# Optimization experiments

Hardware: AMD Instinct MI355X
Metric: run time of the kernel (lower is better)

## Reference

```python
import jax, jax.numpy as jnp
import numpy as np

N = 50000
E = 800000
IN_CH = 128
HID = 32
HEADS = 8
OUT_CH = 64
NEG_SLOPE = 0.2  # PyG GATConv default leaky_relu slope


def setup_inputs() -> dict:
    key = jax.random.key(0)
    ks = jax.random.split(key, 16)
    x = jax.random.normal(ks[0], (N, IN_CH), dtype=jnp.float32)
    edge_index = jax.random.randint(ks[1], (2, E), 0, N, dtype=jnp.int64)
    s = 0.1
    return {
        "x": x,
        "edge_index": edge_index,
        # layer 1: in -> (HEADS, HID), concat
        "W1": jax.random.normal(ks[2], (IN_CH, HEADS * HID), dtype=jnp.float32) * s,
        "att_src1": jax.random.normal(ks[3], (HEADS, HID), dtype=jnp.float32) * s,
        "att_dst1": jax.random.normal(ks[4], (HEADS, HID), dtype=jnp.float32) * s,
        "b1": jnp.zeros((HEADS * HID,), dtype=jnp.float32),
        # layer 2: HEADS*HID -> (HEADS, HID), concat
        "W2": jax.random.normal(ks[5], (HEADS * HID, HEADS * HID), dtype=jnp.float32) * s,
        "att_src2": jax.random.normal(ks[6], (HEADS, HID), dtype=jnp.float32) * s,
        "att_dst2": jax.random.normal(ks[7], (HEADS, HID), dtype=jnp.float32) * s,
        "b2": jnp.zeros((HEADS * HID,), dtype=jnp.float32),
        # layer 3: HEADS*HID -> (1, OUT_CH), no concat (heads=1)
        "W3": jax.random.normal(ks[8], (HEADS * HID, OUT_CH), dtype=jnp.float32) * s,
        "att_src3": jax.random.normal(ks[9], (1, OUT_CH), dtype=jnp.float32) * s,
        "att_dst3": jax.random.normal(ks[10], (1, OUT_CH), dtype=jnp.float32) * s,
        "b3": jnp.zeros((OUT_CH,), dtype=jnp.float32),
    }


def gat_conv(x, src, dst, W, a_src, a_dst, b, heads, ch, concat):
    n = x.shape[0]
    h = (x @ W).reshape(n, heads, ch)                      # [N,H,C]
    alpha_src = jnp.sum(h * a_src, axis=-1)                # [N,H]
    alpha_dst = jnp.sum(h * a_dst, axis=-1)                # [N,H]
    logits = jax.nn.leaky_relu(alpha_src[src] + alpha_dst[dst], NEG_SLOPE)  # [E,H]
    # numerically stable softmax over edges grouped by destination node
    m = jax.ops.segment_max(logits, dst, num_segments=n)   # [N,H]
    m = jnp.where(jnp.isfinite(m), m, 0.0)
    e = jnp.exp(logits - m[dst])                           # [E,H]
    denom = jax.ops.segment_sum(e, dst, num_segments=n)    # [N,H]
    alpha = e / (denom[dst] + 1e-16)                       # [E,H]
    # weighted scatter-aggregate of source features
    out = jax.ops.segment_sum(alpha[:, :, None] * h[src], dst, num_segments=n)  # [N,H,C]
    out = out.reshape(n, heads * ch) if concat else out.mean(axis=1)
    return out + b


def reference(x, edge_index, W1, att_src1, att_dst1, b1,
              W2, att_src2, att_dst2, b2, W3, att_src3, att_dst3, b3):
    src, dst = edge_index[0], edge_index[1]
    h = jax.nn.elu(gat_conv(x, src, dst, W1, att_src1, att_dst1, b1, HEADS, HID, True))
    h = jax.nn.elu(gat_conv(h, src, dst, W2, att_src2, att_dst2, b2, HEADS, HID, True))
    out = gat_conv(h, src, dst, W3, att_src3, att_dst3, b3, 1, OUT_CH, False)
    return out
```

## Files before the change

kernel.cpp:

```cpp
#include <hip/hip_runtime.h>
#include <hip/hip_bf16.h>
#include <hip/hip_fp16.h>
#include <stdint.h>

#define NNODES 50000
#define NEDGES 800000
#define LOG2E 1.44269504088896340736f

typedef float f32x4 __attribute__((ext_vector_type(4)));
typedef _Float16 half8 __attribute__((ext_vector_type(8)));
typedef _Float16 half2v __attribute__((ext_vector_type(2)));

__device__ __forceinline__ ushort f2h(float f) {
  return __half_as_ushort(__float2half(f));
}
__device__ __forceinline__ float2 h2x2(uint32_t u) {
  return __half22float2(__builtin_bit_cast(__half2, u));
}

#if __has_builtin(__builtin_amdgcn_fdot2) && __has_builtin(__builtin_amdgcn_perm) && __has_builtin(__builtin_amdgcn_cvt_pkrtz)
#define USE_DOT2 1
#else
#define USE_DOT2 0
#endif

__device__ __forceinline__ half2v pack2(float a, float b) {
  return __builtin_bit_cast(half2v, __builtin_amdgcn_cvt_pkrtz(a, b));
}

__device__ __forceinline__ float fexp2(float x) {
#if __has_builtin(__builtin_amdgcn_exp2f)
  return __builtin_amdgcn_exp2f(x);
#else
  return exp2f(x);
#endif
}

__device__ __forceinline__ void gload_lds16(const void* g, void* l) {
  __builtin_amdgcn_global_load_lds(
      (const __attribute__((address_space(1))) uint32_t*)g,
      (__attribute__((address_space(3))) uint32_t*)l, 16, 0, 0);
}

__global__ __launch_bounds__(256) void gemm_wide(
    const ushort* __restrict__ A, const ushort* __restrict__ B,
    const float* __restrict__ a_src, const float* __restrict__ a_dst,
    float* __restrict__ as_out, float* __restrict__ ad_out,
    ushort* __restrict__ Cout, int M, int K) {
  __shared__ ushort As[64 * 64];
  __shared__ ushort Bs[256 * 64];

  const int t = threadIdx.x;
  const int w = t >> 6, ln = t & 63;
  const int row0 = blockIdx.x * 64;
  const int wr = (w >> 1) * 32, wc = (w & 1) * 128;

  f32x4 acc[2][8] = {};

  const int nkt = K >> 6;
  for (int kt = 0; kt < nkt; ++kt) {
    const int k0 = kt << 6;
    #pragma unroll
    for (int i = 0; i < 2; ++i) {
      int row8 = w * 2 + i;
      int rloc = row8 * 8 + (ln >> 3);
      int slot = (ln & 7) ^ (rloc & 7);
      int grow = row0 + rloc; grow = grow < M ? grow : M - 1;
      gload_lds16(A + (size_t)grow * K + k0 + slot * 8, As + row8 * 512);
    }
    #pragma unroll
    for (int i = 0; i < 8; ++i) {
      int row8 = w * 8 + i;
      int rloc = row8 * 8 + (ln >> 3);
      int slot = (ln & 7) ^ (rloc & 7);
      gload_lds16(B + (size_t)rloc * K + k0 + slot * 8, Bs + row8 * 512);
    }
    __syncthreads();

    #pragma unroll
    for (int ks = 0; ks < 2; ++ks) {
      half8 a[2], b[8];
      #pragma unroll
      for (int i = 0; i < 2; ++i) {
        int row = wr + i * 16 + (ln & 15);
        int slot = (ks * 4 + (ln >> 4)) ^ (row & 7);
        a[i] = *(const half8*)(As + row * 64 + slot * 8);
      }
      #pragma unroll
      for (int j = 0; j < 8; ++j) {
        int col = wc + j * 16 + (ln & 15);
        int slot = (ks * 4 + (ln >> 4)) ^ (col & 7);
        b[j] = *(const half8*)(Bs + col * 64 + slot * 8);
      }
      #pragma unroll
      for (int i = 0; i < 2; ++i)
        #pragma unroll
        for (int j = 0; j < 8; ++j)
          acc[i][j] = __builtin_amdgcn_mfma_f32_16x16x32_f16(a[i], b[j], acc[i][j], 0, 0, 0);
    }
    __syncthreads();
  }

  const int lx = ln & 15, g = ln >> 4;

  #pragma unroll
  for (int i = 0; i < 2; ++i)
    #pragma unroll
    for (int j = 0; j < 8; ++j)
      #pragma unroll
      for (int r = 0; r < 4; ++r) {
        int grow = row0 + wr + i * 16 + g * 4 + r;
        int gcol = wc + j * 16 + lx;
        if (grow < M) Cout[(size_t)grow * 256 + gcol] = f2h(acc[i][j][r]);
      }

  const int hbase = wc >> 5;
  float avs[8], avd[8];
  #pragma unroll
  for (int j = 0; j < 8; ++j) {
    avs[j] = a_src[wc + j * 16 + lx] * LOG2E;
    avd[j] = a_dst[wc + j * 16 + lx] * LOG2E;
  }
  #pragma unroll
  for (int i = 0; i < 2; ++i)
    #pragma unroll
    for (int r = 0; r < 4; ++r) {
      float ps[4] = {0.f, 0.f, 0.f, 0.f}, pd[4] = {0.f, 0.f, 0.f, 0.f};
      #pragma unroll
      for (int j = 0; j < 8; ++j) {
        float v = acc[i][j][r];
        ps[j >> 1] += v * avs[j];
        pd[j >> 1] += v * avd[j];
      }
      #pragma unroll
      for (int m = 1; m < 16; m <<= 1)
        #pragma unroll
        for (int q = 0; q < 4; ++q) {
          ps[q] += __shfl_xor(ps[q], m);
          pd[q] += __shfl_xor(pd[q], m);
        }
      if (lx == 0) {
        int grow = row0 + wr + i * 16 + g * 4 + r;
        if (grow < M) {
          #pragma unroll
          for (int q = 0; q < 4; ++q) {
            as_out[grow * 8 + hbase + q] = ps[q];
            ad_out[grow * 8 + hbase + q] = pd[q];
          }
        }
      }
    }
}

__global__ __launch_bounds__(256) void gemm_mfma3(
    const ushort* __restrict__ A, const ushort* __restrict__ B,
    const float* __restrict__ a_src, const float* __restrict__ a_dst,
    float* __restrict__ as_out, float* __restrict__ ad_out,
    ushort* __restrict__ Cout, int M, int K, int Ncols) {
  __shared__ ushort As[128 * 64];
  __shared__ ushort Bs[64 * 64];
  __shared__ float redS[2][128], redD[2][128];

  const int t = threadIdx.x;
  const int w = t >> 6, ln = t & 63;
  const int row0 = blockIdx.y * 128;
  const int col0 = blockIdx.x * 64;
  const int wr = (w >> 1) * 64, wc = (w & 1) * 32;

  f32x4 acc[4][2] = {};

  const int nkt = K >> 6;
  for (int kt = 0; kt < nkt; ++kt) {
    const int k0 = kt << 6;
    #pragma unroll
    for (int i = 0; i < 4; ++i) {
      int row8 = w * 4 + i;
      int rloc = row8 * 8 + (ln >> 3);
      int slot = (ln & 7) ^ (rloc & 7);
      int grow = row0 + rloc; grow = grow < M ? grow : M - 1;
      gload_lds16(A + (size_t)grow * K + k0 + slot * 8, As + row8 * 512);
    }
    #pragma unroll
    for (int i = 0; i < 2; ++i) {
      int row8 = w * 2 + i;
      int rloc = row8 * 8 + (ln >> 3);
      int slot = (ln & 7) ^ (rloc & 7);
      gload_lds16(B + (size_t)(col0 + rloc) * K + k0 + slot * 8, Bs + row8 * 512);
    }
    __syncthreads();

    #pragma unroll
    for (int ks = 0; ks < 2; ++ks) {
      half8 a[4], b[2];
      #pragma unroll
      for (int i = 0; i < 4; ++i) {
        int row = wr + i * 16 + (ln & 15);
        int slot = (ks * 4 + (ln >> 4)) ^ (row & 7);
        a[i] = *(const half8*)(As + row * 64 + slot * 8);
      }
      #pragma unroll
      for (int j = 0; j < 2; ++j) {
        int col = wc + j * 16 + (ln & 15);
        int slot = (ks * 4 + (ln >> 4)) ^ (col & 7);
        b[j] = *(const half8*)(Bs + col * 64 + slot * 8);
      }
      #pragma unroll
      for (int i = 0; i < 4; ++i)
        #pragma unroll
        for (int j = 0; j < 2; ++j)
          acc[i][j] = __builtin_amdgcn_mfma_f32_16x16x32_f16(a[i], b[j], acc[i][j], 0, 0, 0);
    }
    __syncthreads();
  }

  const int lx = ln & 15, g = ln >> 4;

  #pragma unroll
  for (int i = 0; i < 4; ++i)
    #pragma unroll
    for (int j = 0; j < 2; ++j)
      #pragma unroll
      for (int r = 0; r < 4; ++r) {
        int grow = row0 + wr + i * 16 + g * 4 + r;
        int gcol = col0 + wc + j * 16 + lx;
        if (grow < M) Cout[(size_t)grow * Ncols + gcol] = f2h(acc[i][j][r]);
      }

  float avs[2], avd[2];
  #pragma unroll
  for (int j = 0; j < 2; ++j) {
    avs[j] = a_src[wc + j * 16 + lx] * LOG2E;
    avd[j] = a_dst[wc + j * 16 + lx] * LOG2E;
  }
  #pragma unroll
  for (int i = 0; i < 4; ++i)
    #pragma unroll
    for (int r = 0; r < 4; ++r) {
      float ps = 0.f, pd = 0.f;
      #pragma unroll
      for (int j = 0; j < 2; ++j) {
        float v = acc[i][j][r];
        ps += v * avs[j];
        pd += v * avd[j];
      }
      #pragma unroll
      for (int m = 1; m < 16; m <<= 1) {
        ps += __shfl_xor(ps, m);
        pd += __shfl_xor(pd, m);
      }
      if (lx == 0) {
        int lrow = wr + i * 16 + g * 4 + r;
        redS[w & 1][lrow] = ps;
        redD[w & 1][lrow] = pd;
      }
    }
  __syncthreads();
  if (t < 128) {
    int grow = row0 + t;
    if (grow < M) {
      as_out[grow] = redS[0][t] + redS[1][t];
      ad_out[grow] = redD[0][t] + redD[1][t];
    }
  }
}

__global__ void cvt_h(const float* __restrict__ in, ushort* __restrict__ out, int n4) {
  int idx = blockIdx.x * blockDim.x + threadIdx.x;
  if (idx >= n4) return;
  float4 v = ((const float4*)in)[idx];
  ushort4 o;
  o.x = f2h(v.x); o.y = f2h(v.y); o.z = f2h(v.z); o.w = f2h(v.w);
  ((ushort4*)out)[idx] = o;
}

__global__ void cvt_w(const float* __restrict__ W, ushort* __restrict__ tr,
                      int K, int N) {
  int idx = blockIdx.x * blockDim.x + threadIdx.x;
  if (idx >= K * N) return;
  int k = idx / N, c = idx - k * N;
  tr[(size_t)c * K + k] = f2h(W[idx]);
}

__global__ void deg_kernel(const int* __restrict__ dst, int* __restrict__ deg, int E) {
  int e = blockIdx.x * blockDim.x + threadIdx.x;
  if (e < E) atomicAdd(&deg[dst[e]], 1);
}

__global__ __launch_bounds__(256) void scan_partial(const int* __restrict__ deg,
                                                    int* __restrict__ rowptr,
                                                    int* __restrict__ blocksum, int n) {
  __shared__ int sdata[256];
  int t = threadIdx.x;
  int base = blockIdx.x * 1024 + t * 4;
  int v[4], s = 0;
  #pragma unroll
  for (int i = 0; i < 4; ++i) {
    v[i] = (base + i < n) ? deg[base + i] : 0;
    s += v[i];
  }
  sdata[t] = s;
  __syncthreads();
  for (int off = 1; off < 256; off <<= 1) {
    int x = (t >= off) ? sdata[t - off] : 0;
    __syncthreads();
    sdata[t] += x;
    __syncthreads();
  }
  int run = sdata[t] - s;
  #pragma unroll
  for (int i = 0; i < 4; ++i) {
    if (base + i < n) rowptr[base + i] = run;
    run += v[i];
  }
  if (t == 255) blocksum[blockIdx.x] = sdata[255];
}

__global__ __launch_bounds__(256) void scan_blocksums(int* __restrict__ blocksum, int nb) {
  __shared__ int sdata[256];
  int t = threadIdx.x;
  int v = (t < nb) ? blocksum[t] : 0;
  sdata[t] = v;
  __syncthreads();
  for (int off = 1; off < 256; off <<= 1) {
    int x = (t >= off) ? sdata[t - off] : 0;
    __syncthreads();
    sdata[t] += x;
    __syncthreads();
  }
  if (t < nb) blocksum[t] = sdata[t] - v;
}

__global__ void scan_add(int* __restrict__ rowptr, const int* __restrict__ blocksum,
                         int* __restrict__ cursor, int n, int E) {
  int idx = blockIdx.x * blockDim.x + threadIdx.x;
  if (idx < n) {
    rowptr[idx] += blocksum[idx >> 10];
    cursor[idx] = 0;
  }
  if (idx == n) rowptr[n] = E;
}

__global__ void scatter_kernel(const int* __restrict__ src, const int* __restrict__ dst,
                               const int* __restrict__ rowptr, int* __restrict__ cursor,
                               int* __restrict__ col_src, int E) {
  int e = blockIdx.x * blockDim.x + threadIdx.x;
  if (e >= E) return;
  int d = dst[e];
  int pos = rowptr[d] + atomicAdd(&cursor[d], 1);
  col_src[pos] = src[e];
}

__global__ __launch_bounds__(256) void aggr_h(
    const int* __restrict__ rowptr, const int* __restrict__ col_src,
    const ushort* __restrict__ h, const float* __restrict__ as_,
    const float* __restrict__ ad_, const float* __restrict__ bias,
    ushort* __restrict__ of, int n) {
  int d = blockIdx.x * 4 + (threadIdx.x >> 6);
  if (d >= n) return;
  int lane = threadIdx.x & 63;
  int c0 = lane * 4;
  int hd = lane >> 3;
  float ad_d = ad_[d * 8 + hd];
  float a0 = 0.f, a1 = 0.f, a2 = 0.f, a3 = 0.f, denom = 0.f;
  const ushort* hp = h + c0;
  int beg = rowptr[d], end = rowptr[d + 1];
  int i = beg;
#if USE_DOT2
  const half2v onepk = {(_Float16)1.f, (_Float16)1.f};
  for (; i + 4 <= end; i += 4) {
    int s0 = col_src[i], s1 = col_src[i + 1], s2 = col_src[i + 2], s3 = col_src[i + 3];
    float l0 = as_[s0 * 8 + hd] + ad_d;
    float l1 = as_[s1 * 8 + hd] + ad_d;
    float l2 = as_[s2 * 8 + hd] + ad_d;
    float l3 = as_[s3 * 8 + hd] + ad_d;
    uint2 v0 = *(const uint2*)(hp + (size_t)s0 * 256);
    uint2 v1 = *(const uint2*)(hp + (size_t)s1 * 256);
    uint2 v2 = *(const uint2*)(hp + (size_t)s2 * 256);
    uint2 v3 = *(const uint2*)(hp + (size_t)s3 * 256);
    float e0 = fexp2(fmaxf(l0, 0.2f * l0));
    float e1 = fexp2(fmaxf(l1, 0.2f * l1));
    float e2 = fexp2(fmaxf(l2, 0.2f * l2));
    float e3 = fexp2(fmaxf(l3, 0.2f * l3));
    half2v ep01 = pack2(e0, e1);
    half2v ep23 = pack2(e2, e3);
    denom = __builtin_amdgcn_fdot2(ep01, onepk, denom, false);
    denom = __builtin_amdgcn_fdot2(ep23, onepk, denom, false);
    uint32_t p;
    p = __builtin_amdgcn_perm(v1.x, v0.x, 0x05040100u);
    a0 = __builtin_amdgcn_fdot2(ep01, __builtin_bit_cast(half2v, p), a0, false);
    p = __builtin_amdgcn_perm(v1.x, v0.x, 0x07060302u);
    a1 = __builtin_amdgcn_fdot2(ep01, __builtin_bit_cast(half2v, p), a1, false);
    p = __builtin_amdgcn_perm(v1.y, v0.y, 0x05040100u);
    a2 = __builtin_amdgcn_fdot2(ep01, __builtin_bit_cast(half2v, p), a2, false);
    p = __builtin_amdgcn_perm(v1.y, v0.y, 0x07060302u);
    a3 = __builtin_amdgcn_fdot2(ep01, __builtin_bit_cast(half2v, p), a3, false);
    p = __builtin_amdgcn_perm(v3.x, v2.x, 0x05040100u);
    a0 = __builtin_amdgcn_fdot2(ep23, __builtin_bit_cast(half2v, p), a0, false);
    p = __builtin_amdgcn_perm(v3.x, v2.x, 0x07060302u);
    a1 = __builtin_amdgcn_fdot2(ep23, __builtin_bit_cast(half2v, p), a1, false);
    p = __builtin_amdgcn_perm(v3.y, v2.y, 0x05040100u);
    a2 = __builtin_amdgcn_fdot2(ep23, __builtin_bit_cast(half2v, p), a2, false);
    p = __builtin_amdgcn_perm(v3.y, v2.y, 0x07060302u);
    a3 = __builtin_amdgcn_fdot2(ep23, __builtin_bit_cast(half2v, p), a3, false);
  }
#endif
  for (; i < end; ++i) {
    int s = col_src[i];
    float l = as_[s * 8 + hd] + ad_d;
    float ev = fexp2(fmaxf(l, 0.2f * l));
    denom += ev;
    uint2 v = *(const uint2*)(hp + (size_t)s * 256);
    float2 p0 = h2x2(v.x), p1 = h2x2(v.y);
    a0 += ev * p0.x;
    a1 += ev * p0.y;
    a2 += ev * p1.x;
    a3 += ev * p1.y;
  }
  float inv = 1.f / (denom + 1e-16f);
  float v0 = a0 * inv + bias[c0 + 0];
  float v1 = a1 * inv + bias[c0 + 1];
  float v2 = a2 * inv + bias[c0 + 2];
  float v3 = a3 * inv + bias[c0 + 3];
  v0 = (v0 > 0.f) ? v0 : expm1f(v0);
  v1 = (v1 > 0.f) ? v1 : expm1f(v1);
  v2 = (v2 > 0.f) ? v2 : expm1f(v2);
  v3 = (v3 > 0.f) ? v3 : expm1f(v3);
  ushort4 hh;
  hh.x = f2h(v0); hh.y = f2h(v1); hh.z = f2h(v2); hh.w = f2h(v3);
  *(ushort4*)(of + (size_t)d * 256 + c0) = hh;
}

__global__ __launch_bounds__(256) void aggr_f3(
    const int* __restrict__ rowptr, const int* __restrict__ col_src,
    const ushort* __restrict__ h, const float* __restrict__ as_,
    const float* __restrict__ ad_, const float* __restrict__ bias,
    float* __restrict__ outp, int n) {
  int wid = (blockIdx.x * 256 + threadIdx.x) >> 6;
  int d = wid * 4 + ((threadIdx.x >> 4) & 3);
  if (d >= n) return;
  int l = threadIdx.x & 15;
  int c0 = l * 4;
  float ad_d = ad_[d];
  float a0 = 0.f, a1 = 0.f, a2 = 0.f, a3 = 0.f, denom = 0.f;
  const ushort* hp = h + c0;
  int beg = rowptr[d], end = rowptr[d + 1];
  int i = beg;
#if USE_DOT2
  const half2v onepk = {(_Float16)1.f, (_Float16)1.f};
  for (; i + 2 <= end; i += 2) {
    int s0 = col_src[i], s1 = col_src[i + 1];
    float l0 = as_[s0] + ad_d;
    float l1 = as_[s1] + ad_d;
    uint2 v0 = *(const uint2*)(hp + (size_t)s0 * 64);
    uint2 v1 = *(const uint2*)(hp + (size_t)s1 * 64);
    float e0 = fexp2(fmaxf(l0, 0.2f * l0));
    float e1 = fexp2(fmaxf(l1, 0.2f * l1));
    half2v ep = pack2(e0, e1);
    denom = __builtin_amdgcn_fdot2(ep, onepk, denom, false);
    uint32_t p;
    p = __builtin_amdgcn_perm(v1.x, v0.x, 0x05040100u);
    a0 = __builtin_amdgcn_fdot2(ep, __builtin_bit_cast(half2v, p), a0, false);
    p = __builtin_amdgcn_perm(v1.x, v0.x, 0x07060302u);
    a1 = __builtin_amdgcn_fdot2(ep, __builtin_bit_cast(half2v, p), a1, false);
    p = __builtin_amdgcn_perm(v1.y, v0.y, 0x05040100u);
    a2 = __builtin_amdgcn_fdot2(ep, __builtin_bit_cast(half2v, p), a2, false);
    p = __builtin_amdgcn_perm(v1.y, v0.y, 0x07060302u);
    a3 = __builtin_amdgcn_fdot2(ep, __builtin_bit_cast(half2v, p), a3, false);
  }
#endif
  for (; i < end; ++i) {
    int s = col_src[i];
    float lg = as_[s] + ad_d;
    float ev = fexp2(fmaxf(lg, 0.2f * lg));
    denom += ev;
    uint2 v = *(const uint2*)(hp + (size_t)s * 64);
    float2 p0 = h2x2(v.x), p1 = h2x2(v.y);
    a0 += ev * p0.x;
    a1 += ev * p0.y;
    a2 += ev * p1.x;
    a3 += ev * p1.y;
  }
  float inv = 1.f / (denom + 1e-16f);
  float4 r;
  r.x = a0 * inv + bias[c0 + 0];
  r.y = a1 * inv + bias[c0 + 1];
  r.z = a2 * inv + bias[c0 + 2];
  r.w = a3 * inv + bias[c0 + 3];
  *(float4*)(outp + (size_t)d * 64 + c0) = r;
}


extern "C" void kernel_launch(void* const* d_in, const int* in_sizes, int n_in,
                              void* d_out, int out_size, void* d_ws, size_t ws_size,
                              hipStream_t stream) {
  const float* x   = (const float*)d_in[0];
  const int*   ei  = (const int*)d_in[1];
  const float* W1  = (const float*)d_in[2];
  const float* aS1 = (const float*)d_in[3];
  const float* aD1 = (const float*)d_in[4];
  const float* b1  = (const float*)d_in[5];
  const float* W2  = (const float*)d_in[6];
  const float* aS2 = (const float*)d_in[7];
  const float* aD2 = (const float*)d_in[8];
  const float* b2  = (const float*)d_in[9];
  const float* W3  = (const float*)d_in[10];
  const float* aS3 = (const float*)d_in[11];
  const float* aD3 = (const float*)d_in[12];
  const float* b3  = (const float*)d_in[13];

  const int* srcp = ei;
  const int* dstp = ei + NEDGES;

  char* base = (char*)d_ws;
  size_t o = 0;
  ushort* hbf  = (ushort*)(base + o); o += 25600000;
  ushort* ff   = (ushort*)(base + o); o += 25600000;
  ushort* f1   = (ushort*)(base + o); o += 12800000;
  float*  as_  = (float*)(base + o);  o += 1600000;
  float*  ad_  = (float*)(base + o);  o += 1600000;
  ushort* w1t  = (ushort*)(base + o); o += 65536;
  ushort* w2t  = (ushort*)(base + o); o += 131072;
  ushort* w3t  = (ushort*)(base + o); o += 32768;
  int* rowptr  = (int*)(base + o);    o += 200016;
  int* cursor  = (int*)(base + o);    o += 200000;
  int* colsrc  = (int*)(base + o);    o += 3200000;
  int* bsum    = (int*)(base + o);    o += 1024;
  float* outp  = (float*)d_out;

  hipMemsetAsync(cursor, 0, NNODES * sizeof(int), stream);
  deg_kernel<<<(NEDGES + 255) / 256, 256, 0, stream>>>(dstp, cursor, NEDGES);
  int nb = (NNODES + 1023) / 1024;
  scan_partial<<<nb, 256, 0, stream>>>(cursor, rowptr, bsum, NNODES);
  scan_blocksums<<<1, 256, 0, stream>>>(bsum, nb);
  scan_add<<<(NNODES + 256) / 256, 256, 0, stream>>>(rowptr, bsum, cursor, NNODES, NEDGES);
  scatter_kernel<<<(NEDGES + 255) / 256, 256, 0, stream>>>(srcp, dstp, rowptr, cursor,
                                                           colsrc, NEDGES);

  cvt_h<<<(NNODES * 128 / 4 + 255) / 256, 256, 0, stream>>>(x, f1, NNODES * 128 / 4);
  cvt_w<<<(128 * 256 + 255) / 256, 256, 0, stream>>>(W1, w1t, 128, 256);
  cvt_w<<<(256 * 256 + 255) / 256, 256, 0, stream>>>(W2, w2t, 256, 256);
  cvt_w<<<(256 * 64 + 255) / 256, 256, 0, stream>>>(W3, w3t, 256, 64);

  const int ga  = (NNODES + 3) / 4;
  const int ga4 = (NNODES + 15) / 16;
  const int gw  = (NNODES + 63) / 64;
  gemm_wide<<<gw, 256, 0, stream>>>(f1, w1t, aS1, aD1, as_, ad_, hbf, NNODES, 128);
  aggr_h<<<ga, 256, 0, stream>>>(rowptr, colsrc, hbf, as_, ad_, b1, ff, NNODES);
  gemm_wide<<<gw, 256, 0, stream>>>(ff, w2t, aS2, aD2, as_, ad_, hbf, NNODES, 256);
  aggr_h<<<ga, 256, 0, stream>>>(rowptr, colsrc, hbf, as_, ad_, b2, ff, NNODES);
  gemm_mfma3<<<dim3(1, (NNODES + 127) / 128), 256, 0, stream>>>(
      ff, w3t, aS3, aD3, as_, ad_, hbf, NNODES, 256, 64);
  aggr_f3<<<ga4, 256, 0, stream>>>(rowptr, colsrc, hbf, as_, ad_, b3, outp, NNODES);
}
```

Baseline: 330.5 us.

## Split attention aggregation into per-head slices with head-major alpha layout

The layer-1/2 aggregation now launches eight blocks per group of nodes, one per head slice. In each wave, 8 lane-groups handle different edges and combine their partial sums with cross-lane shuffles. The attention-score arrays written by the GEMM are stored head-major, so each slice reads a contiguous per-head vector. The three weight-conversion launches are merged into one kernel. The goal is more edge-level parallelism and better cache locality per head, at the cost of reading col_src and rowptr 8 times, doing shuffle reductions, and dropping the fdot2 packed path.

New measurement: 528.1 us. 59.8% more time.

```diff
diff --git a/kernel.cpp b/kernel.cpp
--- a/kernel.cpp
+++ b/kernel.cpp
@@ -144,8 +144,8 @@
         if (grow < M) {
           #pragma unroll
           for (int q = 0; q < 4; ++q) {
-            as_out[grow * 8 + hbase + q] = ps[q];
-            ad_out[grow * 8 + hbase + q] = pd[q];
+            as_out[(size_t)(hbase + q) * M + grow] = ps[q];
+            ad_out[(size_t)(hbase + q) * M + grow] = pd[q];
           }
         }
       }
@@ -273,12 +273,22 @@
   ((ushort4*)out)[idx] = o;
 }
 
-__global__ void cvt_w(const float* __restrict__ W, ushort* __restrict__ tr,
-                      int K, int N) {
+__global__ void cvt_w_all(const float* __restrict__ W1, const float* __restrict__ W2,
+                          const float* __restrict__ W3, ushort* __restrict__ w1t,
+                          ushort* __restrict__ w2t, ushort* __restrict__ w3t) {
   int idx = blockIdx.x * blockDim.x + threadIdx.x;
-  if (idx >= K * N) return;
-  int k = idx / N, c = idx - k * N;
-  tr[(size_t)c * K + k] = f2h(W[idx]);
+  if (idx < 32768) {
+    int k = idx >> 8, c = idx & 255;
+    w1t[(size_t)c * 128 + k] = f2h(W1[idx]);
+  } else if (idx < 32768 + 65536) {
+    int j = idx - 32768;
+    int k = j >> 8, c = j & 255;
+    w2t[(size_t)c * 256 + k] = f2h(W2[j]);
+  } else if (idx < 32768 + 65536 + 16384) {
+    int j = idx - 98304;
+    int k = j >> 6, c = j & 63;
+    w3t[(size_t)c * 256 + k] = f2h(W3[j]);
+  }
 }
 
 __global__ void deg_kernel(const int* __restrict__ dst, int* __restrict__ deg, int E) {
@@ -350,64 +360,27 @@
   col_src[pos] = src[e];
 }
 
-__global__ __launch_bounds__(256) void aggr_h(
+__global__ __launch_bounds__(256) void aggr_slice(
     const int* __restrict__ rowptr, const int* __restrict__ col_src,
     const ushort* __restrict__ h, const float* __restrict__ as_,
     const float* __restrict__ ad_, const float* __restrict__ bias,
     ushort* __restrict__ of, int n) {
-  int d = blockIdx.x * 4 + (threadIdx.x >> 6);
+  int bid = blockIdx.x;
+  int slice = bid & 7;
+  int d = (bid >> 3) * 4 + (threadIdx.x >> 6);
   if (d >= n) return;
   int lane = threadIdx.x & 63;
-  int c0 = lane * 4;
-  int hd = lane >> 3;
-  float ad_d = ad_[d * 8 + hd];
+  int g = lane >> 3;
+  int l = lane & 7;
+  const float* asl = as_ + (size_t)slice * n;
+  float ad_d = ad_[(size_t)slice * n + d];
+  const ushort* hp = h + slice * 32 + l * 4;
   float a0 = 0.f, a1 = 0.f, a2 = 0.f, a3 = 0.f, denom = 0.f;
-  const ushort* hp = h + c0;
   int beg = rowptr[d], end = rowptr[d + 1];
-  int i = beg;
-#if USE_DOT2
-  const half2v onepk = {(_Float16)1.f, (_Float16)1.f};
-  for (; i + 4 <= end; i += 4) {
-    int s0 = col_src[i], s1 = col_src[i + 1], s2 = col_src[i + 2], s3 = col_src[i + 3];
-    float l0 = as_[s0 * 8 + hd] + ad_d;
-    float l1 = as_[s1 * 8 + hd] + ad_d;
-    float l2 = as_[s2 * 8 + hd] + ad_d;
-    float l3 = as_[s3 * 8 + hd] + ad_d;
-    uint2 v0 = *(const uint2*)(hp + (size_t)s0 * 256);
-    uint2 v1 = *(const uint2*)(hp + (size_t)s1 * 256);
-    uint2 v2 = *(const uint2*)(hp + (size_t)s2 * 256);
-    uint2 v3 = *(const uint2*)(hp + (size_t)s3 * 256);
-    float e0 = fexp2(fmaxf(l0, 0.2f * l0));
-    float e1 = fexp2(fmaxf(l1, 0.2f * l1));
-    float e2 = fexp2(fmaxf(l2, 0.2f * l2));
-    float e3 = fexp2(fmaxf(l3, 0.2f * l3));
-    half2v ep01 = pack2(e0, e1);
-    half2v ep23 = pack2(e2, e3);
-    denom = __builtin_amdgcn_fdot2(ep01, onepk, denom, false);
-    denom = __builtin_amdgcn_fdot2(ep23, onepk, denom, false);
-    uint32_t p;
-    p = __builtin_amdgcn_perm(v1.x, v0.x, 0x05040100u);
-    a0 = __builtin_amdgcn_fdot2(ep01, __builtin_bit_cast(half2v, p), a0, false);
-    p = __builtin_amdgcn_perm(v1.x, v0.x, 0x07060302u);
-    a1 = __builtin_amdgcn_fdot2(ep01, __builtin_bit_cast(half2v, p), a1, false);
-    p = __builtin_amdgcn_perm(v1.y, v0.y, 0x05040100u);
-    a2 = __builtin_amdgcn_fdot2(ep01, __builtin_bit_cast(half2v, p), a2, false);
-    p = __builtin_amdgcn_perm(v1.y, v0.y, 0x07060302u);
-    a3 = __builtin_amdgcn_fdot2(ep01, __builtin_bit_cast(half2v, p), a3, false);
-    p = __builtin_amdgcn_perm(v3.x, v2.x, 0x05040100u);
-    a0 = __builtin_amdgcn_fdot2(ep23, __builtin_bit_cast(half2v, p), a0, false);
-    p = __builtin_amdgcn_perm(v3.x, v2.x, 0x07060302u);
-    a1 = __builtin_amdgcn_fdot2(ep23, __builtin_bit_cast(half2v, p), a1, false);
-    p = __builtin_amdgcn_perm(v3.y, v2.y, 0x05040100u);
-    a2 = __builtin_amdgcn_fdot2(ep23, __builtin_bit_cast(half2v, p), a2, false);
-    p = __builtin_amdgcn_perm(v3.y, v2.y, 0x07060302u);
-    a3 = __builtin_amdgcn_fdot2(ep23, __builtin_bit_cast(half2v, p), a3, false);
-  }
-#endif
-  for (; i < end; ++i) {
+  for (int i = beg + g; i < end; i += 8) {
     int s = col_src[i];
-    float l = as_[s * 8 + hd] + ad_d;
-    float ev = fexp2(fmaxf(l, 0.2f * l));
+    float lg = asl[s] + ad_d;
+    float ev = fexp2(fmaxf(lg, 0.2f * lg));
     denom += ev;
     uint2 v = *(const uint2*)(hp + (size_t)s * 256);
     float2 p0 = h2x2(v.x), p1 = h2x2(v.y);
@@ -416,18 +389,29 @@
     a2 += ev * p1.x;
     a3 += ev * p1.y;
   }
-  float inv = 1.f / (denom + 1e-16f);
-  float v0 = a0 * inv + bias[c0 + 0];
-  float v1 = a1 * inv + bias[c0 + 1];
-  float v2 = a2 * inv + bias[c0 + 2];
-  float v3 = a3 * inv + bias[c0 + 3];
-  v0 = (v0 > 0.f) ? v0 : expm1f(v0);
-  v1 = (v1 > 0.f) ? v1 : expm1f(v1);
-  v2 = (v2 > 0.f) ? v2 : expm1f(v2);
-  v3 = (v3 > 0.f) ? v3 : expm1f(v3);
-  ushort4 hh;
-  hh.x = f2h(v0); hh.y = f2h(v1); hh.z = f2h(v2); hh.w = f2h(v3);
-  *(ushort4*)(of + (size_t)d * 256 + c0) = hh;
+  #pragma unroll
+  for (int m = 8; m < 64; m <<= 1) {
+    a0 += __shfl_xor(a0, m);
+    a1 += __shfl_xor(a1, m);
+    a2 += __shfl_xor(a2, m);
+    a3 += __shfl_xor(a3, m);
+    denom += __shfl_xor(denom, m);
+  }
+  if (g == 0) {
+    float inv = 1.f / (denom + 1e-16f);
+    int c0 = slice * 32 + l * 4;
+    float v0 = a0 * inv + bias[c0 + 0];
+    float v1 = a1 * inv + bias[c0 + 1];
+    float v2 = a2 * inv + bias[c0 + 2];
+    float v3 = a3 * inv + bias[c0 + 3];
+    v0 = (v0 > 0.f) ? v0 : expm1f(v0);
+    v1 = (v1 > 0.f) ? v1 : expm1f(v1);
+    v2 = (v2 > 0.f) ? v2 : expm1f(v2);
+    v3 = (v3 > 0.f) ? v3 : expm1f(v3);
+    ushort4 hh;
+    hh.x = f2h(v0); hh.y = f2h(v1); hh.z = f2h(v2); hh.w = f2h(v3);
+    *(ushort4*)(of + (size_t)d * 256 + c0) = hh;
+  }
 }
 
 __global__ __launch_bounds__(256) void aggr_f3(
@@ -537,17 +521,15 @@
                                                            colsrc, NEDGES);
 
   cvt_h<<<(NNODES * 128 / 4 + 255) / 256, 256, 0, stream>>>(x, f1, NNODES * 128 / 4);
-  cvt_w<<<(128 * 256 + 255) / 256, 256, 0, stream>>>(W1, w1t, 128, 256);
-  cvt_w<<<(256 * 256 + 255) / 256, 256, 0, stream>>>(W2, w2t, 256, 256);
-  cvt_w<<<(256 * 64 + 255) / 256, 256, 0, stream>>>(W3, w3t, 256, 64);
-
-  const int ga  = (NNODES + 3) / 4;
+  cvt_w_all<<<(114688 + 255) / 256, 256, 0, stream>>>(W1, W2, W3, w1t, w2t, w3t);
+
+  const int gs  = 8 * ((NNODES + 3) / 4);
   const int ga4 = (NNODES + 15) / 16;
   const int gw  = (NNODES + 63) / 64;
   gemm_wide<<<gw, 256, 0, stream>>>(f1, w1t, aS1, aD1, as_, ad_, hbf, NNODES, 128);
-  aggr_h<<<ga, 256, 0, stream>>>(rowptr, colsrc, hbf, as_, ad_, b1, ff, NNODES);
+  aggr_slice<<<gs, 256, 0, stream>>>(rowptr, colsrc, hbf, as_, ad_, b1, ff, NNODES);
   gemm_wide<<<gw, 256, 0, stream>>>(ff, w2t, aS2, aD2, as_, ad_, hbf, NNODES, 256);
-  aggr_h<<<ga, 256, 0, stream>>>(rowptr, colsrc, hbf, as_, ad_, b2, ff, NNODES);
+  aggr_slice<<<gs, 256, 0, stream>>>(rowptr, colsrc, hbf, as_, ad_, b2, ff, NNODES);
   gemm_mfma3<<<dim3(1, (NNODES + 127) / 128), 256, 0, stream>>>(
       ff, w3t, aS3, aD3, as_, ad_, hbf, NNODES, 256, 64);
   aggr_f3<<<ga4, 256, 0, stream>>>(rowptr, colsrc, hbf, as_, ad_, b3, outp, NNODES);
```

## Split aggr_h edges across half-waves with 16-byte loads; merge weight conversions

Applied to the files above, without the earlier changes.

The layer-1/2 aggregation kernel now gives each half of a wavefront alternate edges of a destination node. Each lane handles 8 channels through 16-byte loads, and the two halves combine their partial sums with a cross-lane shuffle before the epilogue. The intent is more edges in flight per node and wider memory transactions, in exchange for a shuffle reduction and idle lanes during the epilogue. The denominator now accumulates in fp32 instead of through fp16 dot products. Separately, the three weight transpose/convert launches are merged into a single kernel to cut launch overhead.

Result: no change. 324.1 us (-1.9%).

```diff
diff --git a/kernel.cpp b/kernel.cpp
--- a/kernel.cpp
+++ b/kernel.cpp
@@ -10,6 +10,7 @@
 typedef float f32x4 __attribute__((ext_vector_type(4)));
 typedef _Float16 half8 __attribute__((ext_vector_type(8)));
 typedef _Float16 half2v __attribute__((ext_vector_type(2)));
+typedef unsigned short ushort8v __attribute__((ext_vector_type(8)));
 
 __device__ __forceinline__ ushort f2h(float f) {
   return __half_as_ushort(__float2half(f));
@@ -273,12 +274,22 @@
   ((ushort4*)out)[idx] = o;
 }
 
-__global__ void cvt_w(const float* __restrict__ W, ushort* __restrict__ tr,
-                      int K, int N) {
+__global__ void cvt_w_all(const float* __restrict__ W1, const float* __restrict__ W2,
+                          const float* __restrict__ W3, ushort* __restrict__ w1t,
+                          ushort* __restrict__ w2t, ushort* __restrict__ w3t) {
   int idx = blockIdx.x * blockDim.x + threadIdx.x;
-  if (idx >= K * N) return;
-  int k = idx / N, c = idx - k * N;
-  tr[(size_t)c * K + k] = f2h(W[idx]);
+  if (idx < 32768) {
+    int k = idx >> 8, c = idx & 255;
+    w1t[(size_t)c * 128 + k] = f2h(W1[idx]);
+  } else if (idx < 32768 + 65536) {
+    int j = idx - 32768;
+    int k = j >> 8, c = j & 255;
+    w2t[(size_t)c * 256 + k] = f2h(W2[j]);
+  } else if (idx < 32768 + 65536 + 16384) {
+    int j = idx - 98304;
+    int k = j >> 6, c = j & 63;
+    w3t[(size_t)c * 256 + k] = f2h(W3[j]);
+  }
 }
 
 __global__ void deg_kernel(const int* __restrict__ dst, int* __restrict__ deg, int E) {
@@ -358,33 +369,35 @@
   int d = blockIdx.x * 4 + (threadIdx.x >> 6);
   if (d >= n) return;
   int lane = threadIdx.x & 63;
-  int c0 = lane * 4;
-  int hd = lane >> 3;
+  int half = lane >> 5;
+  int l = lane & 31;
+  int c0 = l * 8;
+  int hd = l >> 2;
   float ad_d = ad_[d * 8 + hd];
-  float a0 = 0.f, a1 = 0.f, a2 = 0.f, a3 = 0.f, denom = 0.f;
+  float a0 = 0.f, a1 = 0.f, a2 = 0.f, a3 = 0.f;
+  float a4 = 0.f, a5 = 0.f, a6 = 0.f, a7 = 0.f, denom = 0.f;
   const ushort* hp = h + c0;
   int beg = rowptr[d], end = rowptr[d + 1];
-  int i = beg;
+  int i = beg + half;
 #if USE_DOT2
-  const half2v onepk = {(_Float16)1.f, (_Float16)1.f};
-  for (; i + 4 <= end; i += 4) {
-    int s0 = col_src[i], s1 = col_src[i + 1], s2 = col_src[i + 2], s3 = col_src[i + 3];
+  for (; i + 6 < end; i += 8) {
+    int s0 = col_src[i],     s1 = col_src[i + 2];
+    int s2 = col_src[i + 4], s3 = col_src[i + 6];
     float l0 = as_[s0 * 8 + hd] + ad_d;
     float l1 = as_[s1 * 8 + hd] + ad_d;
     float l2 = as_[s2 * 8 + hd] + ad_d;
     float l3 = as_[s3 * 8 + hd] + ad_d;
-    uint2 v0 = *(const uint2*)(hp + (size_t)s0 * 256);
-    uint2 v1 = *(const uint2*)(hp + (size_t)s1 * 256);
-    uint2 v2 = *(const uint2*)(hp + (size_t)s2 * 256);
-    uint2 v3 = *(const uint2*)(hp + (size_t)s3 * 256);
+    uint4 v0 = *(const uint4*)(hp + (size_t)s0 * 256);
+    uint4 v1 = *(const uint4*)(hp + (size_t)s1 * 256);
+    uint4 v2 = *(const uint4*)(hp + (size_t)s2 * 256);
+    uint4 v3 = *(const uint4*)(hp + (size_t)s3 * 256);
     float e0 = fexp2(fmaxf(l0, 0.2f * l0));
     float e1 = fexp2(fmaxf(l1, 0.2f * l1));
     float e2 = fexp2(fmaxf(l2, 0.2f * l2));
     float e3 = fexp2(fmaxf(l3, 0.2f * l3));
+    denom += (e0 + e1) + (e2 + e3);
     half2v ep01 = pack2(e0, e1);
     half2v ep23 = pack2(e2, e3);
-    denom = __builtin_amdgcn_fdot2(ep01, onepk, denom, false);
-    denom = __builtin_amdgcn_fdot2(ep23, onepk, denom, false);
     uint32_t p;
     p = __builtin_amdgcn_perm(v1.x, v0.x, 0x05040100u);
     a0 = __builtin_amdgcn_fdot2(ep01, __builtin_bit_cast(half2v, p), a0, false);
@@ -394,6 +407,14 @@
     a2 = __builtin_amdgcn_fdot2(ep01, __builtin_bit_cast(half2v, p), a2, false);
     p = __builtin_amdgcn_perm(v1.y, v0.y, 0x07060302u);
     a3 = __builtin_amdgcn_fdot2(ep01, __builtin_bit_cast(half2v, p), a3, false);
+    p = __builtin_amdgcn_perm(v1.z, v0.z, 0x05040100u);
+    a4 = __builtin_amdgcn_fdot2(ep01, __builtin_bit_cast(half2v, p), a4, false);
+    p = __builtin_amdgcn_perm(v1.z, v0.z, 0x07060302u);
+    a5 = __builtin_amdgcn_fdot2(ep01, __builtin_bit_cast(half2v, p), a5, false);
+    p = __builtin_amdgcn_perm(v1.w, v0.w, 0x05040100u);
+    a6 = __builtin_amdgcn_fdot2(ep01, __builtin_bit_cast(half2v, p), a6, false);
+    p = __builtin_amdgcn_perm(v1.w, v0.w, 0x07060302u);
+    a7 = __builtin_amdgcn_fdot2(ep01, __builtin_bit_cast(half2v, p), a7, false);
     p = __builtin_amdgcn_perm(v3.x, v2.x, 0x05040100u);
     a0 = __builtin_amdgcn_fdot2(ep23, __builtin_bit_cast(half2v, p), a0, false);
     p = __builtin_amdgcn_perm(v3.x, v2.x, 0x07060302u);
@@ -402,32 +423,79 @@
     a2 = __builtin_amdgcn_fdot2(ep23, __builtin_bit_cast(half2v, p), a2, false);
     p = __builtin_amdgcn_perm(v3.y, v2.y, 0x07060302u);
     a3 = __builtin_amdgcn_fdot2(ep23, __builtin_bit_cast(half2v, p), a3, false);
+    p = __builtin_amdgcn_perm(v3.z, v2.z, 0x05040100u);
+    a4 = __builtin_amdgcn_fdot2(ep23, __builtin_bit_cast(half2v, p), a4, false);
+    p = __builtin_amdgcn_perm(v3.z, v2.z, 0x07060302u);
+    a5 = __builtin_amdgcn_fdot2(ep23, __builtin_bit_cast(half2v, p), a5, false);
+    p = __builtin_amdgcn_perm(v3.w, v2.w, 0x05040100u);
+    a6 = __builtin_amdgcn_fdot2(ep23, __builtin_bit_cast(half2v, p), a6, false);
+    p = __builtin_amdgcn_perm(v3.w, v2.w, 0x07060302u);
+    a7 = __builtin_amdgcn_fdot2(ep23, __builtin_bit_cast(half2v, p), a7, false);
+  }
+  for (; i + 2 < end; i += 4) {
+    int s0 = col_src[i], s1 = col_src[i + 2];
+    float l0 = as_[s0 * 8 + hd] + ad_d;
+    float l1 = as_[s1 * 8 + hd] + ad_d;
+    uint4 v0 = *(const uint4*)(hp + (size_t)s0 * 256);
+    uint4 v1 = *(const uint4*)(hp + (size_t)s1 * 256);
+    float e0 = fexp2(fmaxf(l0, 0.2f * l0));
+    float e1 = fexp2(fmaxf(l1, 0.2f * l1));
+    denom += e0 + e1;
+    half2v ep = pack2(e0, e1);
+    uint32_t p;
+    p = __builtin_amdgcn_perm(v1.x, v0.x, 0x05040100u);
+    a0 = __builtin_amdgcn_fdot2(ep, __builtin_bit_cast(half2v, p), a0, false);
+    p = __builtin_amdgcn_perm(v1.x, v0.x, 0x07060302u);
+    a1 = __builtin_amdgcn_fdot2(ep, __builtin_bit_cast(half2v, p), a1, false);
+    p = __builtin_amdgcn_perm(v1.y, v0.y, 0x05040100u);
+    a2 = __builtin_amdgcn_fdot2(ep, __builtin_bit_cast(half2v, p), a2, false);
+    p = __builtin_amdgcn_perm(v1.y, v0.y, 0x07060302u);
+    a3 = __builtin_amdgcn_fdot2(ep, __builtin_bit_cast(half2v, p), a3, false);
+    p = __builtin_amdgcn_perm(v1.z, v0.z, 0x05040100u);
+    a4 = __builtin_amdgcn_fdot2(ep, __builtin_bit_cast(half2v, p), a4, false);
+    p = __builtin_amdgcn_perm(v1.z, v0.z, 0x07060302u);
+    a5 = __builtin_amdgcn_fdot2(ep, __builtin_bit_cast(half2v, p), a5, false);
+    p = __builtin_amdgcn_perm(v1.w, v0.w, 0x05040100u);
+    a6 = __builtin_amdgcn_fdot2(ep, __builtin_bit_cast(half2v, p), a6, false);
+    p = __builtin_amdgcn_perm(v1.w, v0.w, 0x07060302u);
+    a7 = __builtin_amdgcn_fdot2(ep, __builtin_bit_cast(half2v, p), a7, false);
   }
 #endif
-  for (; i < end; ++i) {
+  for (; i < end; i += 2) {
     int s = col_src[i];
-    float l = as_[s * 8 + hd] + ad_d;
-    float ev = fexp2(fmaxf(l, 0.2f * l));
+    float lg = as_[s * 8 + hd] + ad_d;
+    float ev = fexp2(fmaxf(lg, 0.2f * lg));
     denom += ev;
-    uint2 v = *(const uint2*)(hp + (size_t)s * 256);
-    float2 p0 = h2x2(v.x), p1 = h2x2(v.y);
-    a0 += ev * p0.x;
-    a1 += ev * p0.y;
-    a2 += ev * p1.x;
-    a3 += ev * p1.y;
-  }
-  float inv = 1.f / (denom + 1e-16f);
-  float v0 = a0 * inv + bias[c0 + 0];
-  float v1 = a1 * inv + bias[c0 + 1];
-  float v2 = a2 * inv + bias[c0 + 2];
-  float v3 = a3 * inv + bias[c0 + 3];
-  v0 = (v0 > 0.f) ? v0 : expm1f(v0);
-  v1 = (v1 > 0.f) ? v1 : expm1f(v1);
-  v2 = (v2 > 0.f) ? v2 : expm1f(v2);
-  v3 = (v3 > 0.f) ? v3 : expm1f(v3);
-  ushort4 hh;
-  hh.x = f2h(v0); hh.y = f2h(v1); hh.z = f2h(v2); hh.w = f2h(v3);
-  *(ushort4*)(of + (size_t)d * 256 + c0) = hh;
+    uint4 v = *(const uint4*)(hp + (size_t)s * 256);
+    float2 p0 = h2x2(v.x), p1 = h2x2(v.y), p2 = h2x2(v.z), p3 = h2x2(v.w);
+    a0 += ev * p0.x; a1 += ev * p0.y;
+    a2 += ev * p1.x; a3 += ev * p1.y;
+    a4 += ev * p2.x; a5 += ev * p2.y;
+    a6 += ev * p3.x; a7 += ev * p3.y;
+  }
+  a0 += __shfl_xor(a0, 32); a1 += __shfl_xor(a1, 32);
+  a2 += __shfl_xor(a2, 32); a3 += __shfl_xor(a3, 32);
+  a4 += __shfl_xor(a4, 32); a5 += __shfl_xor(a5, 32);
+  a6 += __shfl_xor(a6, 32); a7 += __shfl_xor(a7, 32);
+  denom += __shfl_xor(denom, 32);
+  if (half == 0) {
+    float inv = 1.f / (denom + 1e-16f);
+    float4 b0 = *(const float4*)(bias + c0);
+    float4 b1 = *(const float4*)(bias + c0 + 4);
+    float vv[8];
+    vv[0] = a0 * inv + b0.x; vv[1] = a1 * inv + b0.y;
+    vv[2] = a2 * inv + b0.z; vv[3] = a3 * inv + b0.w;
+    vv[4] = a4 * inv + b1.x; vv[5] = a5 * inv + b1.y;
+    vv[6] = a6 * inv + b1.z; vv[7] = a7 * inv + b1.w;
+    ushort8v hh;
+    #pragma unroll
+    for (int j = 0; j < 8; ++j) {
+      float v = vv[j];
+      v = (v > 0.f) ? v : expm1f(v);
+      hh[j] = f2h(v);
+    }
+    *(ushort8v*)(of + (size_t)d * 256 + c0) = hh;
+  }
 }
 
 __global__ __launch_bounds__(256) void aggr_f3(
@@ -537,9 +605,7 @@
                                                            colsrc, NEDGES);
 
   cvt_h<<<(NNODES * 128 / 4 + 255) / 256, 256, 0, stream>>>(x, f1, NNODES * 128 / 4);
-  cvt_w<<<(128 * 256 + 255) / 256, 256, 0, stream>>>(W1, w1t, 128, 256);
-  cvt_w<<<(256 * 256 + 255) / 256, 256, 0, stream>>>(W2, w2t, 256, 256);
-  cvt_w<<<(256 * 64 + 255) / 256, 256, 0, stream>>>(W3, w3t, 256, 64);
+  cvt_w_all<<<(114688 + 255) / 256, 256, 0, stream>>>(W1, W2, W3, w1t, w2t, w3t);
 
   const int ga  = (NNODES + 3) / 4;
   const int ga4 = (NNODES + 15) / 16;
```
